# Kernel optimization log

Hardware: AMD Instinct MI355X
Metric: run time of the kernel (lower is better)

## Reference

```python
import jax, jax.numpy as jnp
import numpy as np

WS = (8, 8)          # window_size
ITER = 1             # iterations
QK_SCALE = 0.17677669529663687  # 32**-0.5


def _l2norm(x, eps=1e-12):
    n = jnp.linalg.norm(x, axis=-1, keepdims=True)
    return x / jnp.maximum(n, eps)


def _get_mask(H, W, onehot, gain=1.0):
    # onehot: [B, h, L, S] cluster assignment weights
    coords = jnp.stack(jnp.meshgrid(jnp.arange(H), jnp.arange(W), indexing='ij'))
    coords = coords.reshape(2, -1).astype(jnp.float32)  # [2, L]
    s = jnp.sum(onehot, axis=-2, keepdims=True)         # [B, h, 1, S]
    s = jnp.where(s == 0, 1.0, s)
    centers = jnp.einsum('cl,bhls->bhcs', coords, onehot) / s  # [B, h, 2, S]
    dh = coords[0][None, None, :, None] - centers[:, :, 0, None, :]  # [B,h,L,S]
    dw = coords[1][None, None, :, None] - centers[:, :, 1, None, :]
    dist = jnp.sqrt(dh * dh + dw * dw)
    return jnp.exp(-dist) * gain  # 1/exp(d) * gain


def setup_inputs() -> dict:
    key = jax.random.key(0)
    k1, k2 = jax.random.split(key)
    B, h, H, W, d = 8, 8, 64, 64, 32
    x_k = jax.random.normal(k1, (B, h, H, W, d), dtype=jnp.float32)
    x_v = jax.random.normal(k2, (B, h, H, W, d), dtype=jnp.float32)
    scale = jnp.asarray(1.0, dtype=jnp.float32)  # nn.Parameter init value
    return {"x_k": x_k, "x_v": x_v, "scale": scale}


def reference(x_k, x_v, scale):
    B, h, H, W, d = x_k.shape
    ws0, ws1 = WS
    H_, W_ = H // ws0, W // ws1
    L, L_ = H * W, H_ * W_

    # initCenter: average pool over non-overlapping windows, then L2 normalize (q only)
    c_q = x_k.reshape(B, h, H_, ws0, W_, ws1, d).mean(axis=(3, 5)).reshape(B, h, L_, d)
    c_q = _l2norm(c_q)

    # initRPE: each pixel assigned to its window index -> one-hot -> coordinate mask
    win_idx = (jnp.arange(H)[:, None] // ws0) * W_ + jnp.arange(W)[None, :] // ws1  # [H, W]
    onehot0 = jax.nn.one_hot(win_idx.reshape(-1), L_, dtype=jnp.float32)[None, None]  # [1,1,L,L_]
    rpb = jnp.broadcast_to(_get_mask(H, W, onehot0), (B, h, L, L_))
    rpb = jax.lax.stop_gradient(rpb)

    xf = x_k.reshape(B, h, L, d)
    aff = None
    for _ in range(ITER):
        # updateCenter: scaled affinity + bias, hard-max mask, softmax, weighted sum, renorm
        aff = jnp.einsum('bhld,bhmd->bhlm', xf * (QK_SCALE * scale), c_q) + rpb
        mx = jnp.max(aff, axis=-1, keepdims=True)
        aff = jax.nn.softmax(jnp.where(aff < mx, -jnp.inf, aff), axis=-1)
        c_q = _l2norm(jnp.einsum('bhlm,bhld->bhmd', aff, xf))
        rpb = jax.lax.stop_gradient(_get_mask(H, W, aff))

    c_v_sum = jnp.einsum('bhlm,bhld->bhmd', aff, x_v.reshape(B, h, L, d))
    a_sum = jnp.sum(aff, axis=-2)[..., None]  # [B, h, L_, 1]
    a_sum = jnp.where(a_sum == 0, 1.0, a_sum)
    c_v = c_v_sum / a_sum
    return (c_q, c_v, rpb)
```

## Files before the change

### kernel.cpp

```cpp
#include <hip/hip_runtime.h>
#include <math.h>


#define NMAPS   64
#define LPIX    4096
#define NCLUS   64
#define DIM     32
#define CHUNKS  8
#define PSTRIDE 4288

__global__ __launch_bounds__(256) void k_initcenter(const float* __restrict__ xk,
                                                    float* __restrict__ cq0) {
    int wid  = threadIdx.x >> 6;
    int lane = threadIdx.x & 63;
    int c    = blockIdx.x * 4 + wid;
    int bh   = c >> 6, m = c & 63;
    int wh   = m >> 3, wc = m & 7;
    int d    = lane & 31, half = lane >> 5;
    const float* base = xk + (size_t)bh * LPIX * DIM;
    float s = 0.f;
#pragma unroll
    for (int k = 0; k < 32; ++k) {
        int pix = k * 2 + half;
        int r = pix >> 3, cc = pix & 7;
        int row = wh * 8 + r, col = wc * 8 + cc;
        s += base[((row << 6) + col) * DIM + d];
    }
    s += __shfl_xor(s, 32);
    float ss = s * s;
#pragma unroll
    for (int o = 16; o >= 1; o >>= 1) ss += __shfl_xor(ss, o);
    float mean = s * (1.0f / 64.0f);
    float norm = sqrtf(ss) * (1.0f / 64.0f);
    float inv  = 1.0f / fmaxf(norm, 1e-12f);
    if (half == 0) cq0[(size_t)c * DIM + d] = mean * inv;
}

__global__ __launch_bounds__(256) void k_rpe0(float* __restrict__ rp0) {
    int g = blockIdx.x * 256 + threadIdx.x;
    int m = g & 63, l = g >> 6;
    float fi = (float)(l >> 6);
    float fj = (float)(l & 63);
    float dh = fi - (float)((m >> 3) * 8) - 3.5f;
    float dw = fj - (float)((m & 7) * 8) - 3.5f;
    rp0[g] = expf(-sqrtf(fmaf(dh, dh, dw * dw)));
}

__global__ __launch_bounds__(512) void k_assign(const float* __restrict__ xk,
                                                const float* __restrict__ xv,
                                                const float* __restrict__ scale,
                                                const float* __restrict__ cq0,
                                                const float* __restrict__ rp0,
                                                float* __restrict__ partial) {
    __shared__ float aq[2][NCLUS * 33];
    __shared__ float av[2][NCLUS * 33];
    __shared__ float as_[2][NCLUS], ach[2][NCLUS], acw[2][NCLUS];

    int t     = threadIdx.x;
    int bh    = blockIdx.x >> 3;
    int chunk = blockIdx.x & (CHUNKS - 1);

    {
        float* aqf = &aq[0][0];
        float* avf = &av[0][0];
        for (int i = t; i < 2 * NCLUS * 33; i += 512) { aqf[i] = 0.f; avf[i] = 0.f; }
        if (t < 2 * NCLUS) { (&as_[0][0])[t] = 0.f; (&ach[0][0])[t] = 0.f; (&acw[0][0])[t] = 0.f; }
    }
    __syncthreads();

    float qs = 0.17677669529663687f * scale[0];
    const float* cqb = cq0 + (size_t)bh * 2048;
    const float* xkb = xk + (size_t)bh * LPIX * DIM;
    const float* xvb = xv + (size_t)bh * LPIX * DIM;

    int l = chunk * 512 + t;
    float fi = (float)(l >> 6);
    float fj = (float)(l & 63);

    float xr[DIM];
    const float4* xp = (const float4*)(xkb + (size_t)l * DIM);
#pragma unroll
    for (int k = 0; k < 8; ++k) {
        float4 v = xp[k];
        xr[k*4] = v.x; xr[k*4+1] = v.y; xr[k*4+2] = v.z; xr[k*4+3] = v.w;
    }

    const float4* rpl = (const float4*)(rp0 + (size_t)l * 64);
    float mx = -INFINITY;
    unsigned long long msk = 0ull;
#pragma unroll
    for (int m4 = 0; m4 < 16; ++m4) {
        float4 r4 = rpl[m4];
        float rj[4] = {r4.x, r4.y, r4.z, r4.w};
#pragma unroll
        for (int j = 0; j < 4; ++j) {
            int m = m4 * 4 + j;
            const float* cm = cqb + m * DIM;
            float dot = 0.f;
#pragma unroll
            for (int k = 0; k < DIM; ++k) dot = fmaf(xr[k], cm[k], dot);
            float val = fmaf(dot, qs, rj[j]);
            if (val > mx)       { mx = val; msk = 1ull << m; }
            else if (val == mx) { msk |= 1ull << m; }
        }
    }
    float w = 1.0f / (float)__popcll(msk);

    float vr[DIM];
    const float4* vp = (const float4*)(xvb + (size_t)l * DIM);
#pragma unroll
    for (int k = 0; k < 8; ++k) {
        float4 v = vp[k];
        vr[k*4] = v.x; vr[k*4+1] = v.y; vr[k*4+2] = v.z; vr[k*4+3] = v.w;
    }

    int rep = t & 1;
    while (msk) {
        int m = __builtin_ctzll(msk);
        msk &= msk - 1;
        float* aqm = &aq[rep][m * 33];
        float* avm = &av[rep][m * 33];
#pragma unroll
        for (int d = 0; d < DIM; ++d) {
            atomicAdd(&aqm[d], w * xr[d]);
            atomicAdd(&avm[d], w * vr[d]);
        }
        atomicAdd(&as_[rep][m], w);
        atomicAdd(&ach[rep][m], w * fi);
        atomicAdd(&acw[rep][m], w * fj);
    }
    __syncthreads();

    float* pw = partial + (size_t)blockIdx.x * PSTRIDE;
    for (int i = t; i < 2048; i += 512) {
        int s = (i >> 5) * 33 + (i & 31);
        pw[i]        = aq[0][s] + aq[1][s];
        pw[2048 + i] = av[0][s] + av[1][s];
    }
    if (t < NCLUS) {
        pw[4096 + t] = as_[0][t] + as_[1][t];
        pw[4160 + t] = ach[0][t] + ach[1][t];
        pw[4224 + t] = acw[0][t] + acw[1][t];
    }
}

__global__ __launch_bounds__(256) void k_reduce(const float* __restrict__ partial,
                                                float* __restrict__ out,
                                                float* __restrict__ cen) {
    __shared__ float sk[2048], sv[2048];
    __shared__ float ss_[NCLUS], sch[NCLUS], scw[NCLUS];
    __shared__ float invq[NCLUS], invv[NCLUS];
    int bh = blockIdx.x, t = threadIdx.x;
    const float* pw = partial + (size_t)bh * CHUNKS * PSTRIDE;

    for (int i = t; i < 2048; i += 256) {
        float a = 0.f, b = 0.f;
#pragma unroll
        for (int p = 0; p < CHUNKS; ++p) {
            a += pw[(size_t)p * PSTRIDE + i];
            b += pw[(size_t)p * PSTRIDE + 2048 + i];
        }
        sk[i] = a; sv[i] = b;
    }
    if (t < NCLUS) {
        float a = 0.f, b = 0.f, c = 0.f;
#pragma unroll
        for (int p = 0; p < CHUNKS; ++p) {
            a += pw[(size_t)p * PSTRIDE + 4096 + t];
            b += pw[(size_t)p * PSTRIDE + 4160 + t];
            c += pw[(size_t)p * PSTRIDE + 4224 + t];
        }
        ss_[t] = a; sch[t] = b; scw[t] = c;
    }
    __syncthreads();
    if (t < NCLUS) {
        float s2 = 0.f;
#pragma unroll
        for (int d = 0; d < DIM; ++d) { float v = sk[t * DIM + d]; s2 = fmaf(v, v, s2); }
        invq[t] = 1.0f / fmaxf(sqrtf(s2), 1e-12f);
        float s  = ss_[t];
        float sp = (s == 0.f) ? 1.f : s;
        invv[t] = 1.0f / sp;
        cen[bh * NCLUS + t]        = sch[t] / sp;
        cen[4096 + bh * NCLUS + t] = scw[t] / sp;
    }
    __syncthreads();
    float* cq = out;
    float* cv = out + 131072;
    for (int i = t; i < 2048; i += 256) {
        int m = i >> 5;
        cq[(size_t)bh * 2048 + i] = sk[i] * invq[m];
        cv[(size_t)bh * 2048 + i] = sv[i] * invv[m];
    }
}

__global__ __launch_bounds__(256) void k_rpb(const float* __restrict__ cen,
                                             float* __restrict__ out) {
    size_t g = (size_t)blockIdx.x * 256 + threadIdx.x;
    int m      = (int)(g & 63);
    size_t lbh = g >> 6;
    int l  = (int)(lbh & 4095);
    int bh = (int)(lbh >> 12);
    float fi = (float)(l >> 6);
    float fj = (float)(l & 63);
    float ch = cen[bh * NCLUS + m];
    float cw = cen[4096 + bh * NCLUS + m];
    float dh = fi - ch, dw = fj - cw;
    out[262144 + g] = expf(-sqrtf(fmaf(dh, dh, dw * dw)));
}

extern "C" void kernel_launch(void* const* d_in, const int* in_sizes, int n_in,
                              void* d_out, int out_size, void* d_ws, size_t ws_size,
                              hipStream_t stream) {
    const float* xk    = (const float*)d_in[0];
    const float* xv    = (const float*)d_in[1];
    const float* scale = (const float*)d_in[2];
    float* out = (float*)d_out;
    float* ws  = (float*)d_ws;

    float* cq0     = ws;
    float* cen     = ws + 131072;
    float* partial = ws + 139264;
    float* rp0     = ws + 139264 + 512 * PSTRIDE;

    k_initcenter<<<1024, 256, 0, stream>>>(xk, cq0);
    k_rpe0<<<1024, 256, 0, stream>>>(rp0);
    k_assign<<<NMAPS * CHUNKS, 512, 0, stream>>>(xk, xv, scale, cq0, rp0, partial);
    k_reduce<<<NMAPS, 256, 0, stream>>>(partial, out, cen);
    k_rpb<<<65536, 256, 0, stream>>>(cen, out);
}
```

Measured before the change: 250.7 us.

## Remap assignment to lane-per-cluster with register accumulation and vectorize rpb writes

The assignment kernel is restructured so each wavefront lane owns one cluster center held in registers. Pixels are staged through shared memory in tiles of eight, and the argmax is computed with wave shuffles and a ballot. Winning lanes accumulate into per-thread registers, which replaces the per-pixel shared atomics with one atomic flush per thread at the end, and the chunk count doubles to keep the grid filled. The rpb output kernel now writes float4 per thread. In exchange the dot products become serialized per pixel across the wave, and most lanes sit idle during accumulation.

```diff
diff --git a/kernel.cpp b/kernel.cpp
--- a/kernel.cpp
+++ b/kernel.cpp
@@ -6,7 +6,7 @@
 #define LPIX    4096
 #define NCLUS   64
 #define DIM     32
-#define CHUNKS  8
+#define CHUNKS  16
 #define PSTRIDE 4288
 
 __global__ __launch_bounds__(256) void k_initcenter(const float* __restrict__ xk,
@@ -46,101 +46,116 @@
     rp0[g] = expf(-sqrtf(fmaf(dh, dh, dw * dw)));
 }
 
-__global__ __launch_bounds__(512) void k_assign(const float* __restrict__ xk,
-                                                const float* __restrict__ xv,
-                                                const float* __restrict__ scale,
-                                                const float* __restrict__ cq0,
-                                                const float* __restrict__ rp0,
-                                                float* __restrict__ partial) {
-    __shared__ float aq[2][NCLUS * 33];
-    __shared__ float av[2][NCLUS * 33];
-    __shared__ float as_[2][NCLUS], ach[2][NCLUS], acw[2][NCLUS];
-
-    int t     = threadIdx.x;
-    int bh    = blockIdx.x >> 3;
+__global__ __launch_bounds__(256, 4) void k_assign(const float* __restrict__ xk,
+                                                   const float* __restrict__ xv,
+                                                   const float* __restrict__ scale,
+                                                   const float* __restrict__ cq0,
+                                                   const float* __restrict__ rp0,
+                                                   float* __restrict__ partial) {
+    __shared__ float sk_[4][256];
+    __shared__ float sv_[4][256];
+    __shared__ float shq[NCLUS * 33];
+    __shared__ float shv[NCLUS * 33];
+    __shared__ float shs[NCLUS], shch[NCLUS], shcw[NCLUS];
+
+    int t    = threadIdx.x;
+    int lane = t & 63;
+    int wid  = t >> 6;
+    int bh    = blockIdx.x >> 4;
     int chunk = blockIdx.x & (CHUNKS - 1);
-
-    {
-        float* aqf = &aq[0][0];
-        float* avf = &av[0][0];
-        for (int i = t; i < 2 * NCLUS * 33; i += 512) { aqf[i] = 0.f; avf[i] = 0.f; }
-        if (t < 2 * NCLUS) { (&as_[0][0])[t] = 0.f; (&ach[0][0])[t] = 0.f; (&acw[0][0])[t] = 0.f; }
-    }
+    int pixbase = chunk * 256 + wid * 64;
+
+    for (int i = t; i < NCLUS * 33; i += 256) { shq[i] = 0.f; shv[i] = 0.f; }
+    if (t < NCLUS) { shs[t] = 0.f; shch[t] = 0.f; shcw[t] = 0.f; }
     __syncthreads();
 
     float qs = 0.17677669529663687f * scale[0];
-    const float* cqb = cq0 + (size_t)bh * 2048;
     const float* xkb = xk + (size_t)bh * LPIX * DIM;
     const float* xvb = xv + (size_t)bh * LPIX * DIM;
 
-    int l = chunk * 512 + t;
-    float fi = (float)(l >> 6);
-    float fj = (float)(l & 63);
-
-    float xr[DIM];
-    const float4* xp = (const float4*)(xkb + (size_t)l * DIM);
-#pragma unroll
-    for (int k = 0; k < 8; ++k) {
-        float4 v = xp[k];
-        xr[k*4] = v.x; xr[k*4+1] = v.y; xr[k*4+2] = v.z; xr[k*4+3] = v.w;
-    }
-
-    const float4* rpl = (const float4*)(rp0 + (size_t)l * 64);
-    float mx = -INFINITY;
-    unsigned long long msk = 0ull;
-#pragma unroll
-    for (int m4 = 0; m4 < 16; ++m4) {
-        float4 r4 = rpl[m4];
-        float rj[4] = {r4.x, r4.y, r4.z, r4.w};
-#pragma unroll
-        for (int j = 0; j < 4; ++j) {
-            int m = m4 * 4 + j;
-            const float* cm = cqb + m * DIM;
+    float c[DIM];
+    {
+        const float4* cp = (const float4*)(cq0 + (size_t)bh * 2048 + lane * DIM);
+#pragma unroll
+        for (int g = 0; g < 8; ++g) {
+            float4 c4 = cp[g];
+            c[g*4] = c4.x; c[g*4+1] = c4.y; c[g*4+2] = c4.z; c[g*4+3] = c4.w;
+        }
+    }
+
+    float accq[DIM], accv[DIM];
+#pragma unroll
+    for (int d = 0; d < DIM; ++d) { accq[d] = 0.f; accv[d] = 0.f; }
+    float s = 0.f, ch = 0.f, cw = 0.f;
+
+    for (int tile = 0; tile < 8; ++tile) {
+        int tp = pixbase + tile * 8;
+        {
+            float4 kk = *(const float4*)(xkb + (size_t)tp * DIM + lane * 4);
+            float4 vv = *(const float4*)(xvb + (size_t)tp * DIM + lane * 4);
+            *(float4*)&sk_[wid][lane * 4] = kk;
+            *(float4*)&sv_[wid][lane * 4] = vv;
+        }
+#pragma unroll
+        for (int i = 0; i < 8; ++i) {
+            int l = tp + i;
+            float fi = (float)(l >> 6);
+            float fj = (float)(l & 63);
+            float rp = rp0[(size_t)l * 64 + lane];
             float dot = 0.f;
 #pragma unroll
-            for (int k = 0; k < DIM; ++k) dot = fmaf(xr[k], cm[k], dot);
-            float val = fmaf(dot, qs, rj[j]);
-            if (val > mx)       { mx = val; msk = 1ull << m; }
-            else if (val == mx) { msk |= 1ull << m; }
-        }
-    }
-    float w = 1.0f / (float)__popcll(msk);
-
-    float vr[DIM];
-    const float4* vp = (const float4*)(xvb + (size_t)l * DIM);
-#pragma unroll
-    for (int k = 0; k < 8; ++k) {
-        float4 v = vp[k];
-        vr[k*4] = v.x; vr[k*4+1] = v.y; vr[k*4+2] = v.z; vr[k*4+3] = v.w;
-    }
-
-    int rep = t & 1;
-    while (msk) {
-        int m = __builtin_ctzll(msk);
-        msk &= msk - 1;
-        float* aqm = &aq[rep][m * 33];
-        float* avm = &av[rep][m * 33];
-#pragma unroll
-        for (int d = 0; d < DIM; ++d) {
-            atomicAdd(&aqm[d], w * xr[d]);
-            atomicAdd(&avm[d], w * vr[d]);
-        }
-        atomicAdd(&as_[rep][m], w);
-        atomicAdd(&ach[rep][m], w * fi);
-        atomicAdd(&acw[rep][m], w * fj);
-    }
+            for (int g = 0; g < 8; ++g) {
+                float4 x4 = *(const float4*)&sk_[wid][i * 32 + g * 4];
+                dot = fmaf(x4.x, c[g*4+0], dot);
+                dot = fmaf(x4.y, c[g*4+1], dot);
+                dot = fmaf(x4.z, c[g*4+2], dot);
+                dot = fmaf(x4.w, c[g*4+3], dot);
+            }
+            float val = fmaf(dot, qs, rp);
+            float mx = val;
+#pragma unroll
+            for (int o = 32; o >= 1; o >>= 1) mx = fmaxf(mx, __shfl_xor(mx, o));
+            unsigned long long ball = __ballot(val == mx);
+            float w = 1.0f / (float)__popcll(ball);
+            if (val == mx) {
+                s += w; ch += w * fi; cw += w * fj;
+#pragma unroll
+                for (int g = 0; g < 8; ++g) {
+                    float4 x4 = *(const float4*)&sk_[wid][i * 32 + g * 4];
+                    float4 v4 = *(const float4*)&sv_[wid][i * 32 + g * 4];
+                    accq[g*4+0] = fmaf(w, x4.x, accq[g*4+0]);
+                    accq[g*4+1] = fmaf(w, x4.y, accq[g*4+1]);
+                    accq[g*4+2] = fmaf(w, x4.z, accq[g*4+2]);
+                    accq[g*4+3] = fmaf(w, x4.w, accq[g*4+3]);
+                    accv[g*4+0] = fmaf(w, v4.x, accv[g*4+0]);
+                    accv[g*4+1] = fmaf(w, v4.y, accv[g*4+1]);
+                    accv[g*4+2] = fmaf(w, v4.z, accv[g*4+2]);
+                    accv[g*4+3] = fmaf(w, v4.w, accv[g*4+3]);
+                }
+            }
+        }
+    }
+
+#pragma unroll
+    for (int d = 0; d < DIM; ++d) {
+        atomicAdd(&shq[lane * 33 + d], accq[d]);
+        atomicAdd(&shv[lane * 33 + d], accv[d]);
+    }
+    atomicAdd(&shs[lane], s);
+    atomicAdd(&shch[lane], ch);
+    atomicAdd(&shcw[lane], cw);
     __syncthreads();
 
     float* pw = partial + (size_t)blockIdx.x * PSTRIDE;
-    for (int i = t; i < 2048; i += 512) {
-        int s = (i >> 5) * 33 + (i & 31);
-        pw[i]        = aq[0][s] + aq[1][s];
-        pw[2048 + i] = av[0][s] + av[1][s];
+    for (int i = t; i < 2048; i += 256) {
+        int sidx = (i >> 5) * 33 + (i & 31);
+        pw[i]        = shq[sidx];
+        pw[2048 + i] = shv[sidx];
     }
     if (t < NCLUS) {
-        pw[4096 + t] = as_[0][t] + as_[1][t];
-        pw[4160 + t] = ach[0][t] + ach[1][t];
-        pw[4224 + t] = acw[0][t] + acw[1][t];
+        pw[4096 + t] = shs[t];
+        pw[4160 + t] = shch[t];
+        pw[4224 + t] = shcw[t];
     }
 }
 
@@ -196,17 +211,21 @@
 
 __global__ __launch_bounds__(256) void k_rpb(const float* __restrict__ cen,
                                              float* __restrict__ out) {
-    size_t g = (size_t)blockIdx.x * 256 + threadIdx.x;
-    int m      = (int)(g & 63);
-    size_t lbh = g >> 6;
-    int l  = (int)(lbh & 4095);
-    int bh = (int)(lbh >> 12);
+    int g4 = blockIdx.x * 256 + threadIdx.x;
+    int mg = (g4 & 15) * 4;
+    int lbh = g4 >> 4;
+    int l  = lbh & 4095;
+    int bh = lbh >> 12;
     float fi = (float)(l >> 6);
     float fj = (float)(l & 63);
-    float ch = cen[bh * NCLUS + m];
-    float cw = cen[4096 + bh * NCLUS + m];
-    float dh = fi - ch, dw = fj - cw;
-    out[262144 + g] = expf(-sqrtf(fmaf(dh, dh, dw * dw)));
+    float4 ch4 = *(const float4*)&cen[bh * 64 + mg];
+    float4 cw4 = *(const float4*)&cen[4096 + bh * 64 + mg];
+    float4 o;
+    { float dh = fi - ch4.x, dw = fj - cw4.x; o.x = expf(-sqrtf(fmaf(dh, dh, dw * dw))); }
+    { float dh = fi - ch4.y, dw = fj - cw4.y; o.y = expf(-sqrtf(fmaf(dh, dh, dw * dw))); }
+    { float dh = fi - ch4.z, dw = fj - cw4.z; o.z = expf(-sqrtf(fmaf(dh, dh, dw * dw))); }
+    { float dh = fi - ch4.w, dw = fj - cw4.w; o.w = expf(-sqrtf(fmaf(dh, dh, dw * dw))); }
+    *(float4*)&out[262144 + (size_t)g4 * 4] = o;
 }
 
 extern "C" void kernel_launch(void* const* d_in, const int* in_sizes, int n_in,
@@ -221,11 +240,11 @@
     float* cq0     = ws;
     float* cen     = ws + 131072;
     float* partial = ws + 139264;
-    float* rp0     = ws + 139264 + 512 * PSTRIDE;
+    float* rp0     = ws + 139264 + 1024 * PSTRIDE;
 
     k_initcenter<<<1024, 256, 0, stream>>>(xk, cq0);
     k_rpe0<<<1024, 256, 0, stream>>>(rp0);
-    k_assign<<<NMAPS * CHUNKS, 512, 0, stream>>>(xk, xv, scale, cq0, rp0, partial);
+    k_assign<<<NMAPS * CHUNKS, 256, 0, stream>>>(xk, xv, scale, cq0, rp0, partial);
     k_reduce<<<NMAPS, 256, 0, stream>>>(partial, out, cen);
-    k_rpb<<<65536, 256, 0, stream>>>(cen, out);
-}
+    k_rpb<<<16384, 256, 0, stream>>>(cen, out);
+}
```

After: 587.1 us. 134% more time.
